# Performance work log

Hardware: AMD Instinct MI355X
Metric: run time of the kernel (lower is better)

Reference implementation:

```python
import jax, jax.numpy as jnp
import numpy as np

N_NODES = 50000
N_EDGES = 800000
NEG_SLOPE = 0.2


def _gat_conv(h, src, dst, W, al, ar, b, res, act):
    """DGL-style GATConv. h:[N,Fin], W:[Fin,H*D], al/ar:[H,D], b:[H*D].
    res: None | [N,H,D] residual value. Returns [N,H,D]."""
    N = h.shape[0]
    H, D = al.shape
    ft = (h @ W).reshape(N, H, D)                       # projected features
    el = jnp.einsum('nhd,hd->nh', ft, al)               # [N,H]
    er = jnp.einsum('nhd,hd->nh', ft, ar)               # [N,H]
    e = jax.nn.leaky_relu(el[src] + er[dst], NEG_SLOPE) # [E,H] edge logits
    # edge softmax over incoming edges of each dst node
    emax = jax.ops.segment_max(e, dst, num_segments=N)  # [N,H]
    emax = jnp.where(jnp.isfinite(emax), emax, 0.0)     # guard empty segments
    ex = jnp.exp(e - emax[dst])                         # [E,H]
    denom = jax.ops.segment_sum(ex, dst, num_segments=N)
    a = ex / denom[dst]                                 # [E,H] attention
    rst = jax.ops.segment_sum(ft[src] * a[..., None], dst, num_segments=N)  # [N,H,D]
    if res is not None:
        rst = rst + res
    rst = rst + b.reshape(1, H, D)
    if act is not None:
        rst = act(rst)
    return rst


def setup_inputs() -> dict:
    key = jax.random.key(0)
    ks = jax.random.split(key, 16)
    s = 0.1
    return {
        'x': jax.random.normal(ks[0], (N_NODES, 128), jnp.float32),
        'edge_src': jax.random.randint(ks[1], (N_EDGES,), 0, N_NODES, jnp.int32),
        'edge_dst': jax.random.randint(ks[2], (N_EDGES,), 0, N_NODES, jnp.int32),
        'W0': jax.random.normal(ks[3], (128, 128), jnp.float32) * s,
        'al0': jax.random.normal(ks[4], (2, 64), jnp.float32) * s,
        'ar0': jax.random.normal(ks[5], (2, 64), jnp.float32) * s,
        'b0': jnp.zeros((128,), jnp.float32),
        'W1': jax.random.normal(ks[6], (128, 128), jnp.float32) * s,
        'al1': jax.random.normal(ks[7], (2, 64), jnp.float32) * s,
        'ar1': jax.random.normal(ks[8], (2, 64), jnp.float32) * s,
        'b1': jnp.zeros((128,), jnp.float32),
        'W2': jax.random.normal(ks[9], (128, 194), jnp.float32) * s,
        'al2': jax.random.normal(ks[10], (2, 97), jnp.float32) * s,
        'ar2': jax.random.normal(ks[11], (2, 97), jnp.float32) * s,
        'b2': jnp.zeros((194,), jnp.float32),
        'res_W2': jax.random.normal(ks[12], (128, 194), jnp.float32) * s,
    }


def reference(x, edge_src, edge_dst, W0, al0, ar0, b0, W1, al1, ar1, b1,
              W2, al2, ar2, b2, res_W2):
    N = x.shape[0]
    elu = jax.nn.elu
    # layer 0: no residual, ELU
    h = _gat_conv(x, edge_src, edge_dst, W0, al0, ar0, b0, None, elu)
    h = h.reshape(N, -1)                                # flatten(1) -> [N,128]
    # layer 1: identity residual (in == heads*out), ELU
    res1 = h.reshape(N, 2, 64)
    h = _gat_conv(h, edge_src, edge_dst, W1, al1, ar1, b1, res1, elu)
    h = h.reshape(N, -1)
    # output layer: linear residual, no activation, mean over heads
    res2 = (h @ res_W2).reshape(N, 2, 97)
    logits = _gat_conv(h, edge_src, edge_dst, W2, al2, ar2, b2, res2, None)
    logits = logits.mean(axis=1)                        # [N, 97]
    # original slices off the last node of each graph (single batched graph)
    return logits[: N - 1]
```

## Files before the change

kernel.cpp:

```cpp
#include <hip/hip_runtime.h>
#include <math.h>

#define NNODES 50000
#define NEDGES 800000
#define NPAD   50048

typedef unsigned int uint;
typedef unsigned short u16;
typedef __bf16 bf16x8 __attribute__((ext_vector_type(8)));
typedef float f32x4 __attribute__((ext_vector_type(4)));

__device__ __forceinline__ float lrelu(float x){ return x > 0.f ? x : 0.2f*x; }
__device__ __forceinline__ float elu_f(float x){ return x > 0.f ? x : expm1f(x); }
__device__ __forceinline__ u16 f2bf(float f){
    uint u = __float_as_uint(f);
    return (u16)((u + 0x7fffu + ((u >> 16) & 1u)) >> 16);
}
__device__ __forceinline__ float bf2f(u16 h){ return __uint_as_float(((uint)h) << 16); }
__device__ __forceinline__ float blo(uint u){ return __uint_as_float(u << 16); }
__device__ __forceinline__ float bhi(uint u){ return __uint_as_float(u & 0xffff0000u); }

__global__ void split_x_bf(const float* __restrict__ x, u16* __restrict__ Xb,
                           u16* __restrict__ H1b, int N)
{
    int idx = blockIdx.x * blockDim.x + threadIdx.x;
    if (idx >= NPAD * 32) return;
    int n = idx >> 5;
    ushort4 hv = make_ushort4(0,0,0,0);
    if (n < N) {
        float4 v = ((const float4*)x)[idx];
        hv.x = f2bf(v.x); hv.y = f2bf(v.y); hv.z = f2bf(v.z); hv.w = f2bf(v.w);
    } else {
        ((ushort4*)H1b)[idx] = make_ushort4(0,0,0,0);
    }
    ((ushort4*)Xb)[idx] = hv;
}

__global__ void split_w_all(const float* __restrict__ W0, const float* __restrict__ W1,
                            const float* __restrict__ W2, const float* __restrict__ Wr,
                            u16* __restrict__ Ball)
{
    int idx = blockIdx.x * blockDim.x + threadIdx.x;
    if (idx >= 768 * 128) return;
    int gcol = idx >> 7, k = idx & 127;
    float v;
    if (gcol < 128)      v = W0[k * 128 + gcol];
    else if (gcol < 256) v = W1[k * 128 + (gcol - 128)];
    else if (gcol < 512) { int c = gcol - 256; v = (c < 194) ? W2[k * 194 + c] : 0.f; }
    else                 { int c = gcol - 512; v = (c < 194) ? Wr[k * 194 + c] : 0.f; }
    Ball[idx] = f2bf(v);
}

__global__ __launch_bounds__(256, 4)
void gemm_l01(const u16* __restrict__ Ab, const u16* __restrict__ Bh, u16* __restrict__ obf,
              const float* __restrict__ alv, const float* __restrict__ arv,
              float* __restrict__ el, float* __restrict__ er, int N)
{
    __shared__ u16 sB[128 * 136];
    const int bm = blockIdx.x * 64;
    const int tid = threadIdx.x, wid = tid >> 6, lane = tid & 63;
    const int lr = lane & 15, q = lane >> 4, lk8 = q << 3;

    bf16x8 aH[4];
    {
        size_t abase = (size_t)(bm + wid*16 + lr) * 128 + lk8;
        #pragma unroll
        for (int kt = 0; kt < 4; kt++)
            aH[kt] = *(const bf16x8*)(Ab + abase + kt*32);
    }
    {
        const int c = tid >> 1, seg = (tid & 1) * 64;
        const u16* g = Bh + (size_t)c * 128 + seg;
        u16* s = sB + c * 136 + seg;
        #pragma unroll
        for (int j = 0; j < 8; j++)
            *(uint4*)(s + j*8) = *(const uint4*)(g + j*8);
    }
    __syncthreads();

    f32x4 acc[8];
    #pragma unroll
    for (int i = 0; i < 8; i++) acc[i] = (f32x4){0.f,0.f,0.f,0.f};

    #pragma unroll
    for (int kt = 0; kt < 4; kt++)
        #pragma unroll
        for (int fs = 0; fs < 8; fs++) {
            bf16x8 b = *(const bf16x8*)(sB + (fs*16 + lr)*136 + kt*32 + lk8);
            acc[fs] = __builtin_amdgcn_mfma_f32_16x16x32_bf16(aH[kt], b, acc[fs], 0, 0, 0);
        }

    float el0[4] = {0,0,0,0}, el1[4] = {0,0,0,0}, er0[4] = {0,0,0,0}, er1[4] = {0,0,0,0};
    #pragma unroll
    for (int fs = 0; fs < 8; fs++) {
        const int col = fs*16 + lr;
        const float av = alv[col], gv = arv[col];
        #pragma unroll
        for (int v = 0; v < 4; v++) {
            float f = acc[fs][v];
            int row = bm + wid*16 + q*4 + v;
            if (row < N) obf[(size_t)row * 128 + col] = f2bf(f);
            if (fs < 4) { el0[v] += f * av; er0[v] += f * gv; }
            else        { el1[v] += f * av; er1[v] += f * gv; }
        }
    }
    #pragma unroll
    for (int off = 1; off < 16; off <<= 1) {
        #pragma unroll
        for (int v = 0; v < 4; v++) {
            el0[v] += __shfl_xor(el0[v], off);
            el1[v] += __shfl_xor(el1[v], off);
            er0[v] += __shfl_xor(er0[v], off);
            er1[v] += __shfl_xor(er1[v], off);
        }
    }
    if (lr == 0) {
        #pragma unroll
        for (int v = 0; v < 4; v++) {
            int row = bm + wid*16 + q*4 + v;
            if (row < N) {
                *(float2*)(el + 2*(size_t)row) = make_float2(el0[v], el1[v]);
                *(float2*)(er + 2*(size_t)row) = make_float2(er0[v], er1[v]);
            }
        }
    }
}

__global__ __launch_bounds__(256, 4)
void gemm_l2(const u16* __restrict__ Ab, const u16* __restrict__ B2, const u16* __restrict__ Br,
             u16* __restrict__ obf, u16* __restrict__ rs2b, int N)
{
    __shared__ u16 sB[128 * 136];
    const int bid = blockIdx.x;
    const int x = (bid >> 5) * 8 + (bid & 7);
    const int sel = (bid >> 3) & 3;
    if (x >= NPAD / 64) return;
    const bool second = (sel >= 2);
    const int coloff = (sel & 1) * 128;
    const u16* __restrict__ B = second ? Br : B2;
    u16* __restrict__ dst = second ? rs2b : obf;

    const int bm = x * 64;
    const int tid = threadIdx.x, wid = tid >> 6, lane = tid & 63;
    const int lr = lane & 15, q = lane >> 4, lk8 = q << 3;

    bf16x8 aH[4];
    {
        size_t abase = (size_t)(bm + wid*16 + lr) * 128 + lk8;
        #pragma unroll
        for (int kt = 0; kt < 4; kt++)
            aH[kt] = *(const bf16x8*)(Ab + abase + kt*32);
    }
    {
        const int c = tid >> 1, seg = (tid & 1) * 64;
        const u16* g = B + (size_t)(coloff + c) * 128 + seg;
        u16* s = sB + c * 136 + seg;
        #pragma unroll
        for (int j = 0; j < 8; j++)
            *(uint4*)(s + j*8) = *(const uint4*)(g + j*8);
    }
    __syncthreads();

    f32x4 acc[8];
    #pragma unroll
    for (int i = 0; i < 8; i++) acc[i] = (f32x4){0.f,0.f,0.f,0.f};

    #pragma unroll
    for (int kt = 0; kt < 4; kt++)
        #pragma unroll
        for (int fs = 0; fs < 8; fs++) {
            bf16x8 b = *(const bf16x8*)(sB + (fs*16 + lr)*136 + kt*32 + lk8);
            acc[fs] = __builtin_amdgcn_mfma_f32_16x16x32_bf16(aH[kt], b, acc[fs], 0, 0, 0);
        }

    #pragma unroll
    for (int fs = 0; fs < 8; fs++) {
        const int col = coloff + fs*16 + lr;
        if (col >= 194) continue;
        #pragma unroll
        for (int v = 0; v < 4; v++) {
            int row = bm + wid*16 + q*4 + v;
            if (row < N) dst[(size_t)row * 194 + col] = f2bf(acc[fs][v]);
        }
    }
}

template<int C, int D>
__global__ void compute_elr(const uint* __restrict__ ftb, const float* __restrict__ al,
                            const float* __restrict__ ar, float* __restrict__ el,
                            float* __restrict__ er, int N)
{
    int wv = threadIdx.x >> 6, lane = threadIdx.x & 63;
    int n = blockIdx.x * 4 + wv;
    if (n >= N) return;
    const uint* row = ftb + (size_t)n * (C/2);
    float l0=0.f, l1=0.f, r0=0.f, r1=0.f;
    for (int p = lane; p < C/2; p += 64) {
        uint u = row[p];
        float f0 = blo(u), f1 = bhi(u);
        int c0 = 2*p, c1 = 2*p + 1;
        float a0 = al[c0], a1 = al[c1], g0 = ar[c0], g1 = ar[c1];
        if (c0 < D) { l0 += f0*a0; r0 += f0*g0; } else { l1 += f0*a0; r1 += f0*g0; }
        if (c1 < D) { l0 += f1*a1; r0 += f1*g1; } else { l1 += f1*a1; r1 += f1*g1; }
    }
    #pragma unroll
    for (int off = 32; off; off >>= 1) {
        l0 += __shfl_down(l0, off); l1 += __shfl_down(l1, off);
        r0 += __shfl_down(r0, off); r1 += __shfl_down(r1, off);
    }
    if (lane == 0) { el[2*n] = l0; el[2*n+1] = l1; er[2*n] = r0; er[2*n+1] = r1; }
}

__global__ void hist_kernel(const int* __restrict__ dst, int* __restrict__ counts, int E)
{
    int i = blockIdx.x * blockDim.x + threadIdx.x;
    if (i < E) atomicAdd(&counts[dst[i]], 1);
}

__global__ __launch_bounds__(1024)
void scan_local(const int* __restrict__ counts, int* __restrict__ row_start,
                int* __restrict__ partials, int n)
{
    __shared__ int wsum[16];
    const int tid = threadIdx.x, lane = tid & 63, wv = tid >> 6;
    const int i0 = blockIdx.x * 4096 + tid * 4;
    int v[4];
    #pragma unroll
    for (int j = 0; j < 4; j++) { int i = i0 + j; v[j] = (i < n) ? counts[i] : 0; }
    v[1] += v[0]; v[2] += v[1]; v[3] += v[2];
    int t = v[3];
    #pragma unroll
    for (int off = 1; off < 64; off <<= 1) {
        int u = __shfl_up(t, off);
        if (lane >= off) t += u;
    }
    int texcl = t - v[3];
    if (lane == 63) wsum[wv] = t;
    __syncthreads();
    int woff = 0;
    for (int w = 0; w < 16; w++) if (w < wv) woff += wsum[w];
    #pragma unroll
    for (int j = 0; j < 4; j++) { int i = i0 + j; if (i < n) row_start[i+1] = woff + texcl + v[j]; }
    if (tid == 0) {
        int tot = 0;
        for (int w = 0; w < 16; w++) tot += wsum[w];
        partials[blockIdx.x] = tot;
    }
}

__global__ void scan_offs(int* __restrict__ partials, int nb)
{
    int lane = threadIdx.x;
    int v = (lane < nb) ? partials[lane] : 0;
    int t = v;
    #pragma unroll
    for (int off = 1; off < 64; off <<= 1) {
        int u = __shfl_up(t, off);
        if (lane >= off) t += u;
    }
    if (lane < nb) partials[lane] = t - v;
}

__global__ __launch_bounds__(1024)
void scan_add(int* __restrict__ row_start, const int* __restrict__ partials, int n)
{
    const int tid = threadIdx.x;
    const int add = partials[blockIdx.x];
    const int i0 = blockIdx.x * 4096 + tid * 4;
    #pragma unroll
    for (int j = 0; j < 4; j++) { int i = i0 + j; if (i < n) row_start[i+1] += add; }
    if (blockIdx.x == 0 && tid == 0) row_start[0] = 0;
}

__global__ void scatter_kernel(const int* __restrict__ src, const int* __restrict__ dst,
                               const int* __restrict__ row_start, int* __restrict__ cursor,
                               int* __restrict__ src_sorted, int E)
{
    int i = blockIdx.x * blockDim.x + threadIdx.x;
    if (i < E) {
        int d = dst[i];
        int p = atomicAdd(&cursor[d], 1);
        src_sorted[row_start[d] + p] = src[i];
    }
}

template<int MODE>
__global__ __launch_bounds__(256)
void gat_agg128(const uint* __restrict__ ftb, const float* __restrict__ el,
                const float* __restrict__ er, const int* __restrict__ row_start,
                const int* __restrict__ ssorted, const u16* __restrict__ Rb,
                const float* __restrict__ bias, u16* __restrict__ Hb)
{
    __shared__ int   s_src[4][64];
    __shared__ float s_w[4][2][64];
    const int wv = threadIdx.x >> 6, lane = threadIdx.x & 63;
    const int n = blockIdx.x * 4 + wv;
    const int beg = row_start[n];
    const int deg = row_start[n+1] - beg;
    const float2 ern = *(const float2*)(er + 2*(size_t)n);
    const int h = lane >> 5;
    float ax = 0.f, ay = 0.f, dp0 = 0.f, dp1 = 0.f;

    for (int cb = 0; cb < deg; cb += 64) {
        const int cnt = min(64, deg - cb);
        float w0 = 0.f, w1 = 0.f; int s = 0;
        if (lane < cnt) {
            s = ssorted[beg + cb + lane];
            float2 e = *(const float2*)(el + 2*(size_t)s);
            w0 = __expf(lrelu(e.x + ern.x));
            w1 = __expf(lrelu(e.y + ern.y));
        }
        dp0 += w0; dp1 += w1;
        s_src[wv][lane] = s; s_w[wv][0][lane] = w0; s_w[wv][1][lane] = w1;
        asm volatile("s_waitcnt lgkmcnt(0)" ::: "memory");
        int t = 0;
        for (; t + 8 <= cnt; t += 8) {
            int4   sa = *(const int4*)&s_src[wv][t];
            int4   sb = *(const int4*)&s_src[wv][t+4];
            float4 wa = *(const float4*)&s_w[wv][h][t];
            float4 wb = *(const float4*)&s_w[wv][h][t+4];
            int   sv[8] = {sa.x,sa.y,sa.z,sa.w,sb.x,sb.y,sb.z,sb.w};
            float wj[8] = {wa.x,wa.y,wa.z,wa.w,wb.x,wb.y,wb.z,wb.w};
            uint U[8];
            #pragma unroll
            for (int j = 0; j < 8; j++) U[j] = ftb[((uint)sv[j] << 6) + lane];
            #pragma unroll
            for (int j = 0; j < 8; j++) { ax += wj[j]*blo(U[j]); ay += wj[j]*bhi(U[j]); }
        }
        for (; t + 4 <= cnt; t += 4) {
            int4   s4 = *(const int4*)&s_src[wv][t];
            float4 w4 = *(const float4*)&s_w[wv][h][t];
            int   sv[4] = {s4.x,s4.y,s4.z,s4.w};
            float wj[4] = {w4.x,w4.y,w4.z,w4.w};
            uint U[4];
            #pragma unroll
            for (int j = 0; j < 4; j++) U[j] = ftb[((uint)sv[j] << 6) + lane];
            #pragma unroll
            for (int j = 0; j < 4; j++) { ax += wj[j]*blo(U[j]); ay += wj[j]*bhi(U[j]); }
        }
        for (; t < cnt; t++) {
            int sv = s_src[wv][t];
            float w = s_w[wv][h][t];
            uint u = ftb[((uint)sv << 6) + lane];
            ax += w*blo(u); ay += w*bhi(u);
        }
    }
    #pragma unroll
    for (int off = 32; off; off >>= 1) { dp0 += __shfl_xor(dp0, off); dp1 += __shfl_xor(dp1, off); }
    const float den = (h == 0) ? dp0 : dp1;
    float r0 = (deg > 0) ? ax / den : 0.f;
    float r1 = (deg > 0) ? ay / den : 0.f;
    const int c0 = 2 * lane;
    const size_t ob = (size_t)n*128 + c0;
    const float2 bv = *(const float2*)(bias + c0);
    float v0 = r0 + bv.x, v1 = r1 + bv.y;
    if (MODE == 1) {
        ushort2 rv = *(const ushort2*)&Rb[ob];
        v0 += bf2f(rv.x);
        v1 += bf2f(rv.y);
    }
    v0 = elu_f(v0); v1 = elu_f(v1);
    *(ushort2*)&Hb[ob] = make_ushort2(f2bf(v0), f2bf(v1));
}

__global__ __launch_bounds__(256)
void gat_agg_out(const uint* __restrict__ ftb, const float* __restrict__ el,
                 const float* __restrict__ er, const int* __restrict__ row_start,
                 const int* __restrict__ ssorted, const u16* __restrict__ resb,
                 const float* __restrict__ bias, float* __restrict__ out)
{
    __shared__ int   s_src[4][64];
    __shared__ float s_w[4][2][64];
    __shared__ float s_a1[4][97];
    const int wv = threadIdx.x >> 6, lane = threadIdx.x & 63;
    const int n = blockIdx.x * 4 + wv;
    if (n >= NNODES - 1) return;
    const int beg = row_start[n];
    const int deg = row_start[n+1] - beg;
    const float2 ern = *(const float2*)(er + 2*(size_t)n);
    const bool dual = (lane < 33);
    const bool xh0 = (lane <= 48), yh0 = (lane <= 47);
    float ax1=0.f, ay1=0.f, ax2=0.f, ay2=0.f, dp0=0.f, dp1=0.f;

    for (int cb = 0; cb < deg; cb += 64) {
        const int cnt = min(64, deg - cb);
        float w0 = 0.f, w1 = 0.f; int s = 0;
        if (lane < cnt) {
            s = ssorted[beg + cb + lane];
            float2 e = *(const float2*)(el + 2*(size_t)s);
            w0 = __expf(lrelu(e.x + ern.x));
            w1 = __expf(lrelu(e.y + ern.y));
        }
        dp0 += w0; dp1 += w1;
        s_src[wv][lane] = s; s_w[wv][0][lane] = w0; s_w[wv][1][lane] = w1;
        asm volatile("s_waitcnt lgkmcnt(0)" ::: "memory");
        int t = 0;
        for (; t + 8 <= cnt; t += 8) {
            int4   sa = *(const int4*)&s_src[wv][t];
            int4   sb = *(const int4*)&s_src[wv][t+4];
            float4 p0a = *(const float4*)&s_w[wv][0][t];
            float4 p0b = *(const float4*)&s_w[wv][0][t+4];
            float4 p1a = *(const float4*)&s_w[wv][1][t];
            float4 p1b = *(const float4*)&s_w[wv][1][t+4];
            int   sv[8] = {sa.x,sa.y,sa.z,sa.w,sb.x,sb.y,sb.z,sb.w};
            float f0[8] = {p0a.x,p0a.y,p0a.z,p0a.w,p0b.x,p0b.y,p0b.z,p0b.w};
            float f1[8] = {p1a.x,p1a.y,p1a.z,p1a.w,p1b.x,p1b.y,p1b.z,p1b.w};
            uint U1[8], U2[8];
            #pragma unroll
            for (int j = 0; j < 8; j++) {
                const uint* row = ftb + (uint)sv[j] * 97u;
                U1[j] = row[lane];
                U2[j] = dual ? row[64 + lane] : 0u;
            }
            #pragma unroll
            for (int j = 0; j < 8; j++) {
                float wx = xh0 ? f0[j] : f1[j], wy = yh0 ? f0[j] : f1[j];
                ax1 += wx*blo(U1[j]); ay1 += wy*bhi(U1[j]);
                ax2 += f1[j]*blo(U2[j]); ay2 += f1[j]*bhi(U2[j]);
            }
        }
        for (; t < cnt; t++) {
            int sv = s_src[wv][t];
            float f0 = s_w[wv][0][t], f1 = s_w[wv][1][t];
            const uint* row = ftb + (uint)sv * 97u;
            uint u1 = row[lane];
            uint u2 = dual ? row[64 + lane] : 0u;
            float wx = xh0 ? f0 : f1, wy = yh0 ? f0 : f1;
            ax1 += wx*blo(u1); ay1 += wy*bhi(u1);
            ax2 += f1*blo(u2); ay2 += f1*bhi(u2);
        }
    }
    #pragma unroll
    for (int off = 32; off; off >>= 1) { dp0 += __shfl_xor(dp0, off); dp1 += __shfl_xor(dp1, off); }
    const float i0 = (deg > 0) ? 1.f/dp0 : 0.f;
    const float i1 = (deg > 0) ? 1.f/dp1 : 0.f;
    float A0x = ax1 * (xh0 ? i0 : i1);
    float A0y = ay1 * (yh0 ? i0 : i1);
    float A2x = ax2 * i1, A2y = ay2 * i1;
    if (lane == 48)      s_a1[wv][0] = A0y;
    else if (lane >= 49) { s_a1[wv][2*lane - 97] = A0x; s_a1[wv][2*lane - 96] = A0y; }
    if (dual)            { s_a1[wv][31 + 2*lane] = A2x; s_a1[wv][32 + 2*lane] = A2y; }
    asm volatile("s_waitcnt lgkmcnt(0)" ::: "memory");
    if (lane <= 48) {
        const int c = 2 * lane;
        const u16* rr = resb + (size_t)n * 194;
        out[(size_t)n*97 + c] = 0.5f*(A0x + s_a1[wv][c] + bf2f(rr[c]) + bf2f(rr[97+c]) + bias[c] + bias[97+c]);
        if (lane < 48)
            out[(size_t)n*97 + c + 1] = 0.5f*(A0y + s_a1[wv][c+1] + bf2f(rr[c+1]) + bf2f(rr[98+c]) + bias[c+1] + bias[98+c]);
    }
}

extern "C" void kernel_launch(void* const* d_in, const int* in_sizes, int n_in,
                              void* d_out, int out_size, void* d_ws, size_t ws_size,
                              hipStream_t stream)
{
    const float* x   = (const float*)d_in[0];
    const int*   esrc= (const int*)  d_in[1];
    const int*   edst= (const int*)  d_in[2];
    const float* W0  = (const float*)d_in[3];
    const float* al0 = (const float*)d_in[4];
    const float* ar0 = (const float*)d_in[5];
    const float* b0  = (const float*)d_in[6];
    const float* W1  = (const float*)d_in[7];
    const float* al1 = (const float*)d_in[8];
    const float* ar1 = (const float*)d_in[9];
    const float* b1  = (const float*)d_in[10];
    const float* W2  = (const float*)d_in[11];
    const float* al2 = (const float*)d_in[12];
    const float* ar2 = (const float*)d_in[13];
    const float* b2  = (const float*)d_in[14];
    const float* rW2 = (const float*)d_in[15];
    float* out = (float*)d_out;

    const int N = NNODES, E = NEDGES;
    const int NB = (N + 4095) / 4096;
    float* ws = (float*)d_ws;
    size_t o = 0;
    auto alloc_f = [&](size_t count) { float* p = ws + o; o += (count + 3) & ~(size_t)3; return p; };
    float* el   = alloc_f((size_t)N * 2);
    float* er   = alloc_f((size_t)N * 2);
    uint*  ftb  = (uint*)alloc_f((size_t)N * 97);
    u16*   rs2b = (u16*)alloc_f((size_t)N * 97);
    u16*   Xb   = (u16*)alloc_f((size_t)NPAD * 64);
    u16*   H1b  = (u16*)alloc_f((size_t)NPAD * 64);
    u16*   Ball = (u16*)alloc_f(768 * 64);
    int* row_start = (int*)alloc_f(N + 4);
    int* cursor    = (int*)alloc_f(N);
    int* partials  = (int*)alloc_f(64);
    int* ssorted   = (int*)alloc_f(E);
    u16* B0h = Ball, *B1h = Ball + 128*128, *B2h = Ball + 256*128, *Brh = Ball + 512*128;

    hipMemsetAsync(cursor, 0, N * sizeof(int), stream);
    hist_kernel<<<(E + 255) / 256, 256, 0, stream>>>(edst, cursor, E);
    scan_local<<<NB, 1024, 0, stream>>>(cursor, row_start, partials, N);
    scan_offs<<<1, 64, 0, stream>>>(partials, NB);
    scan_add<<<NB, 1024, 0, stream>>>(row_start, partials, N);
    hipMemsetAsync(cursor, 0, N * sizeof(int), stream);
    scatter_kernel<<<(E + 255) / 256, 256, 0, stream>>>(esrc, edst, row_start, cursor, ssorted, E);

    split_x_bf<<<NPAD * 32 / 256, 256, 0, stream>>>(x, Xb, H1b, N);
    split_w_all<<<768 * 128 / 256, 256, 0, stream>>>(W0, W1, W2, rW2, Ball);

    const int gx = NPAD / 64;
    const int agg_grid = N / 4;
    const int elr_grid = (N + 3) / 4;

    gemm_l01<<<gx, 256, 0, stream>>>(Xb, B0h, (u16*)ftb, al0, ar0, el, er, N);
    gat_agg128<0><<<agg_grid, 256, 0, stream>>>(ftb, el, er, row_start, ssorted, nullptr, b0, H1b);

    gemm_l01<<<gx, 256, 0, stream>>>(H1b, B1h, (u16*)ftb, al1, ar1, el, er, N);
    gat_agg128<1><<<agg_grid, 256, 0, stream>>>(ftb, el, er, row_start, ssorted, H1b, b1, Xb);

    gemm_l2<<<((gx + 7) / 8) * 32, 256, 0, stream>>>(Xb, B2h, Brh, (u16*)ftb, rs2b, N);
    compute_elr<194,97><<<elr_grid, 256, 0, stream>>>(ftb, al2, ar2, el, er, N);
    gat_agg_out<<<agg_grid, 256, 0, stream>>>(ftb, el, er, row_start, ssorted, rs2b, b2, out);
}
```

Measured before the change: 310.4 us.

## Aggregate before projecting in output GAT layer and fuse scan and prep kernels

The output layer now aggregates the 128-wide hidden features per head and applies the projection afterwards, using linearity. One GEMM over the concatenated [agg_h0, agg_h1, h] input then applies W2, the residual weights and the head mean. The attention logits for layer 2 use precomputed W2·al and W2·ar vectors and are computed inside the layer-1 aggregation epilogue, which removes the compute_elr pass and the 194-wide gathers. The three-kernel scan becomes a single decoupled-lookback scan that also writes the scatter cursors, and the prep kernels are merged into one. This adds a spin-wait dependency between scan blocks and drops the 4-wide remainder loop in gat_agg128.

Result: faster. 297.0 us (-4.3%).

```diff
diff --git a/kernel.cpp b/kernel.cpp
--- a/kernel.cpp
+++ b/kernel.cpp
@@ -20,35 +20,59 @@
 __device__ __forceinline__ float blo(uint u){ return __uint_as_float(u << 16); }
 __device__ __forceinline__ float bhi(uint u){ return __uint_as_float(u & 0xffff0000u); }
 
-__global__ void split_x_bf(const float* __restrict__ x, u16* __restrict__ Xb,
-                           u16* __restrict__ H1b, int N)
+#define R0 (NPAD*32)
+#define R1 (R0 + 256*128)
+#define R2 (R1 + 128*384)
+#define R3 (R2 + 256)
+#define R4 (R3 + 128)
+__global__ void prep_all(const float* __restrict__ x,
+                         const float* __restrict__ W0, const float* __restrict__ W1,
+                         const float* __restrict__ W2, const float* __restrict__ Wr,
+                         const float* __restrict__ al2, const float* __restrict__ ar2,
+                         const float* __restrict__ b2,
+                         u16* __restrict__ Xb, u16* __restrict__ H1b,
+                         u16* __restrict__ B01, u16* __restrict__ Bf,
+                         float* __restrict__ alp2, float* __restrict__ arp2,
+                         float* __restrict__ cb, int N)
 {
     int idx = blockIdx.x * blockDim.x + threadIdx.x;
-    if (idx >= NPAD * 32) return;
-    int n = idx >> 5;
-    ushort4 hv = make_ushort4(0,0,0,0);
-    if (n < N) {
-        float4 v = ((const float4*)x)[idx];
-        hv.x = f2bf(v.x); hv.y = f2bf(v.y); hv.z = f2bf(v.z); hv.w = f2bf(v.w);
-    } else {
-        ((ushort4*)H1b)[idx] = make_ushort4(0,0,0,0);
-    }
-    ((ushort4*)Xb)[idx] = hv;
-}
-
-__global__ void split_w_all(const float* __restrict__ W0, const float* __restrict__ W1,
-                            const float* __restrict__ W2, const float* __restrict__ Wr,
-                            u16* __restrict__ Ball)
-{
-    int idx = blockIdx.x * blockDim.x + threadIdx.x;
-    if (idx >= 768 * 128) return;
-    int gcol = idx >> 7, k = idx & 127;
-    float v;
-    if (gcol < 128)      v = W0[k * 128 + gcol];
-    else if (gcol < 256) v = W1[k * 128 + (gcol - 128)];
-    else if (gcol < 512) { int c = gcol - 256; v = (c < 194) ? W2[k * 194 + c] : 0.f; }
-    else                 { int c = gcol - 512; v = (c < 194) ? Wr[k * 194 + c] : 0.f; }
-    Ball[idx] = f2bf(v);
+    if (idx < R0) {
+        int n = idx >> 5;
+        ushort4 hv = make_ushort4(0,0,0,0);
+        if (n < N) {
+            float4 v = ((const float4*)x)[idx];
+            hv.x = f2bf(v.x); hv.y = f2bf(v.y); hv.z = f2bf(v.z); hv.w = f2bf(v.w);
+        } else {
+            ((ushort4*)H1b)[idx] = make_ushort4(0,0,0,0);
+        }
+        ((ushort4*)Xb)[idx] = hv;
+    } else if (idx < R1) {
+        int j = idx - R0, gcol = j >> 7, k = j & 127;
+        float v = (gcol < 128) ? W0[k*128 + gcol] : W1[k*128 + (gcol - 128)];
+        B01[j] = f2bf(v);
+    } else if (idx < R2) {
+        int j = idx - R1, c = j / 384, k = j - c*384;
+        float v = 0.f;
+        if (c < 97) {
+            if (k < 128)      v = W2[k*194 + c];
+            else if (k < 256) v = W2[(k-128)*194 + 97 + c];
+            else              v = Wr[(k-256)*194 + c] + Wr[(k-256)*194 + 97 + c];
+        }
+        Bf[c*384 + k] = f2bf(v);
+    } else if (idx < R3) {
+        int t = idx - R2, k = t & 127, h = t >> 7;
+        float sl = 0.f, sr = 0.f;
+        for (int d = 0; d < 97; d++) {
+            float w = W2[k*194 + h*97 + d];
+            sl += w * al2[h*97 + d];
+            sr += w * ar2[h*97 + d];
+        }
+        alp2[h*128 + k] = sl;
+        arp2[h*128 + k] = sr;
+    } else if (idx < R4) {
+        int c = idx - R3;
+        if (c < 97) cb[c] = 0.5f * (b2[c] + b2[97 + c]);
+    }
 }
 
 __global__ __launch_bounds__(256, 4)
@@ -126,89 +150,65 @@
     }
 }
 
-__global__ __launch_bounds__(256, 4)
-void gemm_l2(const u16* __restrict__ Ab, const u16* __restrict__ B2, const u16* __restrict__ Br,
-             u16* __restrict__ obf, u16* __restrict__ rs2b, int N)
-{
-    __shared__ u16 sB[128 * 136];
+__global__ __launch_bounds__(256, 3)
+void gemm_final(const u16* __restrict__ agg01, const u16* __restrict__ h2b,
+                const u16* __restrict__ Bf, const float* __restrict__ cb,
+                float* __restrict__ out, int N)
+{
+    __shared__ u16 sB[64 * 392];
     const int bid = blockIdx.x;
-    const int x = (bid >> 5) * 8 + (bid & 7);
-    const int sel = (bid >> 3) & 3;
+    const int x = (bid >> 4) * 8 + (bid & 7);
+    const int ct = (bid >> 3) & 1;
     if (x >= NPAD / 64) return;
-    const bool second = (sel >= 2);
-    const int coloff = (sel & 1) * 128;
-    const u16* __restrict__ B = second ? Br : B2;
-    u16* __restrict__ dst = second ? rs2b : obf;
-
     const int bm = x * 64;
     const int tid = threadIdx.x, wid = tid >> 6, lane = tid & 63;
     const int lr = lane & 15, q = lane >> 4, lk8 = q << 3;
 
-    bf16x8 aH[4];
+    bf16x8 aF[12];
     {
-        size_t abase = (size_t)(bm + wid*16 + lr) * 128 + lk8;
+        const int row = bm + wid*16 + lr;
+        const u16* pa = agg01 + (size_t)row * 256;
+        #pragma unroll
+        for (int kt = 0; kt < 8; kt++)
+            aF[kt] = *(const bf16x8*)(pa + kt*32 + lk8);
+        const u16* ph = h2b + (size_t)row * 128;
         #pragma unroll
         for (int kt = 0; kt < 4; kt++)
-            aH[kt] = *(const bf16x8*)(Ab + abase + kt*32);
+            aF[8 + kt] = *(const bf16x8*)(ph + kt*32 + lk8);
     }
     {
-        const int c = tid >> 1, seg = (tid & 1) * 64;
-        const u16* g = B + (size_t)(coloff + c) * 128 + seg;
-        u16* s = sB + c * 136 + seg;
-        #pragma unroll
-        for (int j = 0; j < 8; j++)
+        const int c = tid >> 2, seg = (tid & 3) * 96;
+        const u16* g = Bf + (size_t)(ct*64 + c) * 384 + seg;
+        u16* s = sB + c * 392 + seg;
+        #pragma unroll
+        for (int j = 0; j < 12; j++)
             *(uint4*)(s + j*8) = *(const uint4*)(g + j*8);
     }
     __syncthreads();
 
-    f32x4 acc[8];
-    #pragma unroll
-    for (int i = 0; i < 8; i++) acc[i] = (f32x4){0.f,0.f,0.f,0.f};
-
-    #pragma unroll
-    for (int kt = 0; kt < 4; kt++)
-        #pragma unroll
-        for (int fs = 0; fs < 8; fs++) {
-            bf16x8 b = *(const bf16x8*)(sB + (fs*16 + lr)*136 + kt*32 + lk8);
-            acc[fs] = __builtin_amdgcn_mfma_f32_16x16x32_bf16(aH[kt], b, acc[fs], 0, 0, 0);
-        }
-
-    #pragma unroll
-    for (int fs = 0; fs < 8; fs++) {
-        const int col = coloff + fs*16 + lr;
-        if (col >= 194) continue;
+    f32x4 acc[4];
+    #pragma unroll
+    for (int i = 0; i < 4; i++) acc[i] = (f32x4){0.f,0.f,0.f,0.f};
+
+    #pragma unroll
+    for (int kt = 0; kt < 12; kt++)
+        #pragma unroll
+        for (int fs = 0; fs < 4; fs++) {
+            bf16x8 b = *(const bf16x8*)(sB + (fs*16 + lr)*392 + kt*32 + lk8);
+            acc[fs] = __builtin_amdgcn_mfma_f32_16x16x32_bf16(aF[kt], b, acc[fs], 0, 0, 0);
+        }
+
+    #pragma unroll
+    for (int fs = 0; fs < 4; fs++) {
+        const int col = ct*64 + fs*16 + lr;
+        if (col >= 97) continue;
+        const float cbc = cb[col];
         #pragma unroll
         for (int v = 0; v < 4; v++) {
             int row = bm + wid*16 + q*4 + v;
-            if (row < N) dst[(size_t)row * 194 + col] = f2bf(acc[fs][v]);
-        }
-    }
-}
-
-template<int C, int D>
-__global__ void compute_elr(const uint* __restrict__ ftb, const float* __restrict__ al,
-                            const float* __restrict__ ar, float* __restrict__ el,
-                            float* __restrict__ er, int N)
-{
-    int wv = threadIdx.x >> 6, lane = threadIdx.x & 63;
-    int n = blockIdx.x * 4 + wv;
-    if (n >= N) return;
-    const uint* row = ftb + (size_t)n * (C/2);
-    float l0=0.f, l1=0.f, r0=0.f, r1=0.f;
-    for (int p = lane; p < C/2; p += 64) {
-        uint u = row[p];
-        float f0 = blo(u), f1 = bhi(u);
-        int c0 = 2*p, c1 = 2*p + 1;
-        float a0 = al[c0], a1 = al[c1], g0 = ar[c0], g1 = ar[c1];
-        if (c0 < D) { l0 += f0*a0; r0 += f0*g0; } else { l1 += f0*a0; r1 += f0*g0; }
-        if (c1 < D) { l0 += f1*a1; r0 += f1*g1; } else { l1 += f1*a1; r1 += f1*g1; }
-    }
-    #pragma unroll
-    for (int off = 32; off; off >>= 1) {
-        l0 += __shfl_down(l0, off); l1 += __shfl_down(l1, off);
-        r0 += __shfl_down(r0, off); r1 += __shfl_down(r1, off);
-    }
-    if (lane == 0) { el[2*n] = l0; el[2*n+1] = l1; er[2*n] = r0; er[2*n+1] = r1; }
+            if (row < N - 1) out[(size_t)row * 97 + col] = 0.5f * acc[fs][v] + cbc;
+        }
+    }
 }
 
 __global__ void hist_kernel(const int* __restrict__ dst, int* __restrict__ counts, int E)
@@ -218,16 +218,17 @@
 }
 
 __global__ __launch_bounds__(1024)
-void scan_local(const int* __restrict__ counts, int* __restrict__ row_start,
-                int* __restrict__ partials, int n)
+void scan_dl(int* __restrict__ cnt_cur, int* __restrict__ row_start,
+             int* __restrict__ flags, int* __restrict__ prefixes, int n)
 {
     __shared__ int wsum[16];
+    __shared__ int sExc;
     const int tid = threadIdx.x, lane = tid & 63, wv = tid >> 6;
     const int i0 = blockIdx.x * 4096 + tid * 4;
-    int v[4];
-    #pragma unroll
-    for (int j = 0; j < 4; j++) { int i = i0 + j; v[j] = (i < n) ? counts[i] : 0; }
-    v[1] += v[0]; v[2] += v[1]; v[3] += v[2];
+    int c[4], v[4];
+    #pragma unroll
+    for (int j = 0; j < 4; j++) { int i = i0 + j; c[j] = (i < n) ? cnt_cur[i] : 0; }
+    v[0] = c[0]; v[1] = v[0] + c[1]; v[2] = v[1] + c[2]; v[3] = v[2] + c[3];
     int t = v[3];
     #pragma unroll
     for (int off = 1; off < 64; off <<= 1) {
@@ -237,50 +238,43 @@
     int texcl = t - v[3];
     if (lane == 63) wsum[wv] = t;
     __syncthreads();
-    int woff = 0;
-    for (int w = 0; w < 16; w++) if (w < wv) woff += wsum[w];
-    #pragma unroll
-    for (int j = 0; j < 4; j++) { int i = i0 + j; if (i < n) row_start[i+1] = woff + texcl + v[j]; }
     if (tid == 0) {
         int tot = 0;
+        #pragma unroll
         for (int w = 0; w < 16; w++) tot += wsum[w];
-        partials[blockIdx.x] = tot;
-    }
-}
-
-__global__ void scan_offs(int* __restrict__ partials, int nb)
-{
-    int lane = threadIdx.x;
-    int v = (lane < nb) ? partials[lane] : 0;
-    int t = v;
-    #pragma unroll
-    for (int off = 1; off < 64; off <<= 1) {
-        int u = __shfl_up(t, off);
-        if (lane >= off) t += u;
-    }
-    if (lane < nb) partials[lane] = t - v;
-}
-
-__global__ __launch_bounds__(1024)
-void scan_add(int* __restrict__ row_start, const int* __restrict__ partials, int n)
-{
-    const int tid = threadIdx.x;
-    const int add = partials[blockIdx.x];
-    const int i0 = blockIdx.x * 4096 + tid * 4;
-    #pragma unroll
-    for (int j = 0; j < 4; j++) { int i = i0 + j; if (i < n) row_start[i+1] += add; }
-    if (blockIdx.x == 0 && tid == 0) row_start[0] = 0;
+        int exc = 0;
+        if (blockIdx.x > 0) {
+            while (atomicAdd(&flags[blockIdx.x - 1], 0) == 0) __builtin_amdgcn_s_sleep(2);
+            exc = atomicAdd(&prefixes[blockIdx.x - 1], 0);
+        } else {
+            row_start[0] = 0;
+        }
+        atomicExch(&prefixes[blockIdx.x], exc + tot);
+        __threadfence();
+        atomicExch(&flags[blockIdx.x], 1);
+        sExc = exc;
+    }
+    __syncthreads();
+    int woff = sExc + texcl;
+    for (int w = 0; w < 16; w++) if (w < wv) woff += wsum[w];
+    #pragma unroll
+    for (int j = 0; j < 4; j++) {
+        int i = i0 + j;
+        if (i < n) {
+            int inc = woff + v[j];
+            row_start[i + 1] = inc;
+            cnt_cur[i] = inc - c[j];
+        }
+    }
 }
 
 __global__ void scatter_kernel(const int* __restrict__ src, const int* __restrict__ dst,
-                               const int* __restrict__ row_start, int* __restrict__ cursor,
-                               int* __restrict__ src_sorted, int E)
+                               int* __restrict__ cursor, int* __restrict__ src_sorted, int E)
 {
     int i = blockIdx.x * blockDim.x + threadIdx.x;
     if (i < E) {
-        int d = dst[i];
-        int p = atomicAdd(&cursor[d], 1);
-        src_sorted[row_start[d] + p] = src[i];
+        int p = atomicAdd(&cursor[dst[i]], 1);
+        src_sorted[p] = src[i];
     }
 }
 
@@ -289,7 +283,9 @@
 void gat_agg128(const uint* __restrict__ ftb, const float* __restrict__ el,
                 const float* __restrict__ er, const int* __restrict__ row_start,
                 const int* __restrict__ ssorted, const u16* __restrict__ Rb,
-                const float* __restrict__ bias, u16* __restrict__ Hb)
+                const float* __restrict__ bias, u16* __restrict__ Hb,
+                const float* __restrict__ alp2, const float* __restrict__ arp2,
+                float* __restrict__ el2, float* __restrict__ er2)
 {
     __shared__ int   s_src[4][64];
     __shared__ float s_w[4][2][64];
@@ -327,17 +323,6 @@
             #pragma unroll
             for (int j = 0; j < 8; j++) { ax += wj[j]*blo(U[j]); ay += wj[j]*bhi(U[j]); }
         }
-        for (; t + 4 <= cnt; t += 4) {
-            int4   s4 = *(const int4*)&s_src[wv][t];
-            float4 w4 = *(const float4*)&s_w[wv][h][t];
-            int   sv[4] = {s4.x,s4.y,s4.z,s4.w};
-            float wj[4] = {w4.x,w4.y,w4.z,w4.w};
-            uint U[4];
-            #pragma unroll
-            for (int j = 0; j < 4; j++) U[j] = ftb[((uint)sv[j] << 6) + lane];
-            #pragma unroll
-            for (int j = 0; j < 4; j++) { ax += wj[j]*blo(U[j]); ay += wj[j]*bhi(U[j]); }
-        }
         for (; t < cnt; t++) {
             int sv = s_src[wv][t];
             float w = s_w[wv][h][t];
@@ -361,26 +346,41 @@
     }
     v0 = elu_f(v0); v1 = elu_f(v1);
     *(ushort2*)&Hb[ob] = make_ushort2(f2bf(v0), f2bf(v1));
+
+    if constexpr (MODE == 1) {
+        float2 a0 = *(const float2*)(alp2 + c0);
+        float2 a1 = *(const float2*)(alp2 + 128 + c0);
+        float2 g0 = *(const float2*)(arp2 + c0);
+        float2 g1 = *(const float2*)(arp2 + 128 + c0);
+        float e0 = v0*a0.x + v1*a0.y;
+        float e1 = v0*a1.x + v1*a1.y;
+        float f0 = v0*g0.x + v1*g0.y;
+        float f1 = v0*g1.x + v1*g1.y;
+        #pragma unroll
+        for (int off = 32; off; off >>= 1) {
+            e0 += __shfl_xor(e0, off); e1 += __shfl_xor(e1, off);
+            f0 += __shfl_xor(f0, off); f1 += __shfl_xor(f1, off);
+        }
+        if (lane == 0) {
+            *(float2*)(el2 + 2*(size_t)n) = make_float2(e0, e1);
+            *(float2*)(er2 + 2*(size_t)n) = make_float2(f0, f1);
+        }
+    }
 }
 
 __global__ __launch_bounds__(256)
-void gat_agg_out(const uint* __restrict__ ftb, const float* __restrict__ el,
-                 const float* __restrict__ er, const int* __restrict__ row_start,
-                 const int* __restrict__ ssorted, const u16* __restrict__ resb,
-                 const float* __restrict__ bias, float* __restrict__ out)
+void gat_agg_out2(const uint* __restrict__ h2u, const float* __restrict__ el,
+                  const float* __restrict__ er, const int* __restrict__ row_start,
+                  const int* __restrict__ ssorted, u16* __restrict__ agg01)
 {
     __shared__ int   s_src[4][64];
     __shared__ float s_w[4][2][64];
-    __shared__ float s_a1[4][97];
     const int wv = threadIdx.x >> 6, lane = threadIdx.x & 63;
     const int n = blockIdx.x * 4 + wv;
-    if (n >= NNODES - 1) return;
     const int beg = row_start[n];
     const int deg = row_start[n+1] - beg;
     const float2 ern = *(const float2*)(er + 2*(size_t)n);
-    const bool dual = (lane < 33);
-    const bool xh0 = (lane <= 48), yh0 = (lane <= 47);
-    float ax1=0.f, ay1=0.f, ax2=0.f, ay2=0.f, dp0=0.f, dp1=0.f;
+    float ax0 = 0.f, ay0 = 0.f, ax1 = 0.f, ay1 = 0.f, dp0 = 0.f, dp1 = 0.f;
 
     for (int cb = 0; cb < deg; cb += 64) {
         const int cnt = min(64, deg - cb);
@@ -405,49 +405,32 @@
             int   sv[8] = {sa.x,sa.y,sa.z,sa.w,sb.x,sb.y,sb.z,sb.w};
             float f0[8] = {p0a.x,p0a.y,p0a.z,p0a.w,p0b.x,p0b.y,p0b.z,p0b.w};
             float f1[8] = {p1a.x,p1a.y,p1a.z,p1a.w,p1b.x,p1b.y,p1b.z,p1b.w};
-            uint U1[8], U2[8];
+            uint U[8];
+            #pragma unroll
+            for (int j = 0; j < 8; j++) U[j] = h2u[((uint)sv[j] << 6) + lane];
             #pragma unroll
             for (int j = 0; j < 8; j++) {
-                const uint* row = ftb + (uint)sv[j] * 97u;
-                U1[j] = row[lane];
-                U2[j] = dual ? row[64 + lane] : 0u;
-            }
-            #pragma unroll
-            for (int j = 0; j < 8; j++) {
-                float wx = xh0 ? f0[j] : f1[j], wy = yh0 ? f0[j] : f1[j];
-                ax1 += wx*blo(U1[j]); ay1 += wy*bhi(U1[j]);
-                ax2 += f1[j]*blo(U2[j]); ay2 += f1[j]*bhi(U2[j]);
+                float lo = blo(U[j]), hi = bhi(U[j]);
+                ax0 += f0[j]*lo; ay0 += f0[j]*hi;
+                ax1 += f1[j]*lo; ay1 += f1[j]*hi;
             }
         }
         for (; t < cnt; t++) {
             int sv = s_src[wv][t];
             float f0 = s_w[wv][0][t], f1 = s_w[wv][1][t];
-            const uint* row = ftb + (uint)sv * 97u;
-            uint u1 = row[lane];
-            uint u2 = dual ? row[64 + lane] : 0u;
-            float wx = xh0 ? f0 : f1, wy = yh0 ? f0 : f1;
-            ax1 += wx*blo(u1); ay1 += wy*bhi(u1);
-            ax2 += f1*blo(u2); ay2 += f1*bhi(u2);
+            uint u = h2u[((uint)sv << 6) + lane];
+            float lo = blo(u), hi = bhi(u);
+            ax0 += f0*lo; ay0 += f0*hi;
+            ax1 += f1*lo; ay1 += f1*hi;
         }
     }
     #pragma unroll
     for (int off = 32; off; off >>= 1) { dp0 += __shfl_xor(dp0, off); dp1 += __shfl_xor(dp1, off); }
     const float i0 = (deg > 0) ? 1.f/dp0 : 0.f;
     const float i1 = (deg > 0) ? 1.f/dp1 : 0.f;
-    float A0x = ax1 * (xh0 ? i0 : i1);
-    float A0y = ay1 * (yh0 ? i0 : i1);
-    float A2x = ax2 * i1, A2y = ay2 * i1;
-    if (lane == 48)      s_a1[wv][0] = A0y;
-    else if (lane >= 49) { s_a1[wv][2*lane - 97] = A0x; s_a1[wv][2*lane - 96] = A0y; }
-    if (dual)            { s_a1[wv][31 + 2*lane] = A2x; s_a1[wv][32 + 2*lane] = A2y; }
-    asm volatile("s_waitcnt lgkmcnt(0)" ::: "memory");
-    if (lane <= 48) {
-        const int c = 2 * lane;
-        const u16* rr = resb + (size_t)n * 194;
-        out[(size_t)n*97 + c] = 0.5f*(A0x + s_a1[wv][c] + bf2f(rr[c]) + bf2f(rr[97+c]) + bias[c] + bias[97+c]);
-        if (lane < 48)
-            out[(size_t)n*97 + c + 1] = 0.5f*(A0y + s_a1[wv][c+1] + bf2f(rr[c+1]) + bf2f(rr[98+c]) + bias[c+1] + bias[98+c]);
-    }
+    const int c0 = 2 * lane;
+    *(ushort2*)&agg01[(size_t)n*256 + c0]       = make_ushort2(f2bf(ax0*i0), f2bf(ay0*i0));
+    *(ushort2*)&agg01[(size_t)n*256 + 128 + c0] = make_ushort2(f2bf(ax1*i1), f2bf(ay1*i1));
 }
 
 extern "C" void kernel_launch(void* const* d_in, const int* in_sizes, int n_in,
@@ -477,41 +460,44 @@
     float* ws = (float*)d_ws;
     size_t o = 0;
     auto alloc_f = [&](size_t count) { float* p = ws + o; o += (count + 3) & ~(size_t)3; return p; };
-    float* el   = alloc_f((size_t)N * 2);
-    float* er   = alloc_f((size_t)N * 2);
-    uint*  ftb  = (uint*)alloc_f((size_t)N * 97);
-    u16*   rs2b = (u16*)alloc_f((size_t)N * 97);
-    u16*   Xb   = (u16*)alloc_f((size_t)NPAD * 64);
-    u16*   H1b  = (u16*)alloc_f((size_t)NPAD * 64);
-    u16*   Ball = (u16*)alloc_f(768 * 64);
+    float* el    = alloc_f((size_t)N * 2);
+    float* er    = alloc_f((size_t)N * 2);
+    float* el2   = alloc_f((size_t)N * 2);
+    float* er2   = alloc_f((size_t)N * 2);
+    uint*  ftb   = (uint*)alloc_f((size_t)N * 64);
+    u16*   agg01 = (u16*)alloc_f((size_t)NPAD * 128);
+    u16*   Xb    = (u16*)alloc_f((size_t)NPAD * 64);
+    u16*   H1b   = (u16*)alloc_f((size_t)NPAD * 64);
+    u16*   B01   = (u16*)alloc_f(256 * 64);
+    u16*   Bf    = (u16*)alloc_f(128 * 192);
+    float* alp2  = alloc_f(256);
+    float* arp2  = alloc_f(256);
+    float* cbv   = alloc_f(128);
     int* row_start = (int*)alloc_f(N + 4);
-    int* cursor    = (int*)alloc_f(N);
-    int* partials  = (int*)alloc_f(64);
+    int* cursor    = (int*)alloc_f(N + 64);
+    int* flags     = cursor + N;
+    int* prefixes  = cursor + N + 16;
     int* ssorted   = (int*)alloc_f(E);
-    u16* B0h = Ball, *B1h = Ball + 128*128, *B2h = Ball + 256*128, *Brh = Ball + 512*128;
-
-    hipMemsetAsync(cursor, 0, N * sizeof(int), stream);
+
+    hipMemsetAsync(cursor, 0, (N + 64) * sizeof(int), stream);
     hist_kernel<<<(E + 255) / 256, 256, 0, stream>>>(edst, cursor, E);
-    scan_local<<<NB, 1024, 0, stream>>>(cursor, row_start, partials, N);
-    scan_offs<<<1, 64, 0, stream>>>(partials, NB);
-    scan_add<<<NB, 1024, 0, stream>>>(row_start, partials, N);
-    hipMemsetAsync(cursor, 0, N * sizeof(int), stream);
-    scatter_kernel<<<(E + 255) / 256, 256, 0, stream>>>(esrc, edst, row_start, cursor, ssorted, E);
-
-    split_x_bf<<<NPAD * 32 / 256, 256, 0, stream>>>(x, Xb, H1b, N);
-    split_w_all<<<768 * 128 / 256, 256, 0, stream>>>(W0, W1, W2, rW2, Ball);
+    scan_dl<<<NB, 1024, 0, stream>>>(cursor, row_start, flags, prefixes, N);
+    scatter_kernel<<<(E + 255) / 256, 256, 0, stream>>>(esrc, edst, cursor, ssorted, E);
+
+    prep_all<<<(R4 + 255) / 256, 256, 0, stream>>>(x, W0, W1, W2, rW2, al2, ar2, b2,
+                                                   Xb, H1b, B01, Bf, alp2, arp2, cbv, N);
 
     const int gx = NPAD / 64;
     const int agg_grid = N / 4;
-    const int elr_grid = (N + 3) / 4;
-
-    gemm_l01<<<gx, 256, 0, stream>>>(Xb, B0h, (u16*)ftb, al0, ar0, el, er, N);
-    gat_agg128<0><<<agg_grid, 256, 0, stream>>>(ftb, el, er, row_start, ssorted, nullptr, b0, H1b);
-
-    gemm_l01<<<gx, 256, 0, stream>>>(H1b, B1h, (u16*)ftb, al1, ar1, el, er, N);
-    gat_agg128<1><<<agg_grid, 256, 0, stream>>>(ftb, el, er, row_start, ssorted, H1b, b1, Xb);
-
-    gemm_l2<<<((gx + 7) / 8) * 32, 256, 0, stream>>>(Xb, B2h, Brh, (u16*)ftb, rs2b, N);
-    compute_elr<194,97><<<elr_grid, 256, 0, stream>>>(ftb, al2, ar2, el, er, N);
-    gat_agg_out<<<agg_grid, 256, 0, stream>>>(ftb, el, er, row_start, ssorted, rs2b, b2, out);
-}
+
+    gemm_l01<<<gx, 256, 0, stream>>>(Xb, B01, (u16*)ftb, al0, ar0, el, er, N);
+    gat_agg128<0><<<agg_grid, 256, 0, stream>>>(ftb, el, er, row_start, ssorted,
+                                                nullptr, b0, H1b, nullptr, nullptr, nullptr, nullptr);
+
+    gemm_l01<<<gx, 256, 0, stream>>>(H1b, B01 + 128*128, (u16*)ftb, al1, ar1, el, er, N);
+    gat_agg128<1><<<agg_grid, 256, 0, stream>>>(ftb, el, er, row_start, ssorted,
+                                                H1b, b1, Xb, alp2, arp2, el2, er2);
+
+    gat_agg_out2<<<agg_grid, 256, 0, stream>>>((uint*)Xb, el2, er2, row_start, ssorted, agg01);
+    gemm_final<<<((gx + 7) / 8) * 16, 256, 0, stream>>>(agg01, Xb, Bf, cbv, out, N);
+}
```
